# Kernel tuning notes

Measured on AMD Instinct MI355X. Metric: run time of the kernel, lower is better.

## Reference

```python
import jax, jax.numpy as jnp
import numpy as np

NUM_HEADS = 6
TAU = 1.0


def _split_heads(y, h):
    b, n, c = y.shape
    return y.reshape(b, n, h, c // h).transpose(0, 2, 1, 3)  # b h n d


def setup_inputs() -> dict:
    key = jax.random.key(0)
    B, M, C = 8, 1026, 384
    names = ["Wq1", "Wq2", "Wk1", "Wk2", "Wv1", "Wv2", "Wo"]
    ks = jax.random.split(key, len(names) + 3)
    inp = {"x": jax.random.normal(ks[0], (B, M, C), jnp.float32)}
    for i, nm in enumerate(names):
        inp[nm] = jax.random.normal(ks[i + 1], (C, C), jnp.float32) * 0.02
        inp["b" + nm[1:]] = jnp.zeros((C,), jnp.float32)
    inp["weights"] = jax.random.normal(ks[-2], (4,), jnp.float32)
    u = jax.random.uniform(ks[-1], (4,), jnp.float32, 1e-6, 1.0 - 1e-6)
    inp["gumbel_noise"] = -jnp.log(-jnp.log(u))  # fixed gumbel sample for determinism
    return inp


def reference(x, Wq1, bq1, Wq2, bq2, Wk1, bk1, Wk2, bk2,
              Wv1, bv1, Wv2, bv2, Wo, bo, weights, gumbel_noise):
    B, M, C = x.shape
    N1 = (M - 2) // 2 + 1  # N + 1, quadrant size
    h = NUM_HEADS
    d = C // h
    scale = d ** -0.5
    x1, x2 = x[:, :N1], x[:, N1:]
    q = jnp.concatenate([_split_heads(x1 @ Wq1 + bq1, h),
                         _split_heads(x2 @ Wq2 + bq2, h)], axis=2)  # b h M d
    k = jnp.concatenate([_split_heads(x1 @ Wk1 + bk1, h),
                         _split_heads(x2 @ Wk2 + bk2, h)], axis=2)
    v1 = _split_heads(x1 @ Wv1 + bv1, h)  # b h N1 d
    v2 = _split_heads(x2 @ Wv2 + bv2, h)
    attn = jnp.einsum('bhqd,bhkd->bhqk', q, k) * scale  # b h M M
    b1 = jax.nn.softmax(attn[:, :, :N1, :N1], axis=-1)
    b2 = jax.nn.softmax(attn[:, :, :N1, N1:], axis=-1)
    b3 = jax.nn.softmax(attn[:, :, N1:, :N1], axis=-1)
    b4 = jax.nn.softmax(attn[:, :, N1:, N1:], axis=-1)
    # hard gumbel-softmax gate (straight-through)
    y_soft = jax.nn.softmax((weights + gumbel_noise) / TAU)
    y_hard = jax.nn.one_hot(jnp.argmax(y_soft), 4, dtype=y_soft.dtype)
    w = y_hard + y_soft - jax.lax.stop_gradient(y_soft)
    A = w[0] * b1 + w[1] * b2 + w[2] * b3 + w[3] * b4  # b h N1 N1
    out1 = jnp.einsum('bhqk,bhkd->bhqd', A, v1)
    out2 = jnp.einsum('bhqk,bhkd->bhqd', A, v2)
    out = jnp.concatenate([out1, out2], axis=2)  # b h M d
    out = out.transpose(0, 2, 1, 3).reshape(B, M, C)
    return out @ Wo + bo
```

## Files before the change

kernel.cpp:

```cpp
#include <hip/hip_runtime.h>

typedef unsigned short u16;
typedef short v8s __attribute__((ext_vector_type(8)));
typedef float v4f __attribute__((ext_vector_type(4)));

namespace {
constexpr int kC = 384;
constexpr int kN1 = 513;
constexpr int kH = 6;
constexpr int kBH = 48;
constexpr int kRows = 4104;
constexpr int kRows2 = 8208;
constexpr int kPld = 576;
}

__device__ __forceinline__ u16 f2b(float f) {
  unsigned int u = __float_as_uint(f);
  u += 0x7fffu + ((u >> 16) & 1u);
  return (u16)(u >> 16);
}

__device__ __forceinline__ int gumbel_argmax(const float* __restrict__ w,
                                             const float* __restrict__ g) {
  float v0 = w[0] + g[0], v1 = w[1] + g[1], v2 = w[2] + g[2], v3 = w[3] + g[3];
  int j = 0;
  float m = v0;
  if (v1 > m) { m = v1; j = 1; }
  if (v2 > m) { m = v2; j = 2; }
  if (v3 > m) { m = v3; j = 3; }
  return j;
}

__global__ __launch_bounds__(256) void prep_w(
    const float* __restrict__ Wq1, const float* __restrict__ Wq2,
    const float* __restrict__ Wk1, const float* __restrict__ Wk2,
    const float* __restrict__ Wv1, const float* __restrict__ Wv2,
    const float* __restrict__ Wo, const float* __restrict__ wts,
    const float* __restrict__ gum, u16* __restrict__ Wqt,
    u16* __restrict__ Wkt, u16* __restrict__ Wv1t, u16* __restrict__ Wv2t,
    u16* __restrict__ Wot) {
  __shared__ float tb[32][33];
  const int bx = blockIdx.x;
  const int z = bx / 144, rem = bx - z * 144;
  const int c0 = (rem % 12) * 32, r0 = (rem / 12) * 32;
  const int j = gumbel_argmax(wts, gum);
  const float* src;
  u16* dst;
  switch (z) {
    case 0: src = (j < 2) ? Wq1 : Wq2; dst = Wqt; break;
    case 1: src = (j == 0 || j == 2) ? Wk1 : Wk2; dst = Wkt; break;
    case 2: src = Wv1; dst = Wv1t; break;
    case 3: src = Wv2; dst = Wv2t; break;
    default: src = Wo; dst = Wot; break;
  }
  const int tx = threadIdx.x & 31, ty = threadIdx.x >> 5;
  for (int p = 0; p < 4; ++p)
    tb[ty + p * 8][tx] = src[(size_t)(r0 + ty + p * 8) * kC + c0 + tx];
  __syncthreads();
  for (int p = 0; p < 4; ++p)
    dst[(size_t)(c0 + ty + p * 8) * kC + r0 + tx] = f2b(tb[tx][ty + p * 8]);
}

__global__ __launch_bounds__(256) void qkv_mfma(
    const float* __restrict__ x, const u16* __restrict__ Wqt,
    const u16* __restrict__ Wkt, const u16* __restrict__ Wv1t,
    const u16* __restrict__ Wv2t, const float* __restrict__ bq1,
    const float* __restrict__ bq2, const float* __restrict__ bk1,
    const float* __restrict__ bk2, const float* __restrict__ bv1,
    const float* __restrict__ bv2, const float* __restrict__ wts,
    const float* __restrict__ gum, u16* __restrict__ Qb, u16* __restrict__ Kb,
    u16* __restrict__ Vt1, u16* __restrict__ Vt2) {
  __shared__ __align__(16) u16 As[128][72];
  __shared__ __align__(16) u16 Bs[128][72];
  const int op = blockIdx.z;
  const int j = gumbel_argmax(wts, gum);
  const bool vmode = (op >= 2);
  const float* bias;
  int xoff;
  const u16* Wt;
  if (op == 0) {
    bias = (j < 2) ? bq1 : bq2; xoff = (j < 2) ? 0 : kN1; Wt = Wqt;
  } else if (op == 1) {
    const bool u1 = (j == 0 || j == 2);
    bias = u1 ? bk1 : bk2; xoff = u1 ? 0 : kN1; Wt = Wkt;
  } else if (op == 2) {
    bias = bv1; xoff = 0; Wt = Wv1t;
  } else {
    bias = bv2; xoff = kN1; Wt = Wv2t;
  }
  const int mb = vmode ? blockIdx.y : blockIdx.x;
  const int nb = vmode ? blockIdx.x : blockIdx.y;
  const int m0 = mb * 128, n0 = nb * 128;
  const int tid = threadIdx.x;
  const int lane = tid & 63, l16 = lane & 15, quad = lane >> 4;
  const int wv = tid >> 6, wr = wv >> 1, wc = wv & 1;
  const int sr = tid >> 2, sc = (tid & 3) * 16;

  v4f acc[4][4];
  const v4f z4 = {0.f, 0.f, 0.f, 0.f};
  for (int i = 0; i < 4; ++i)
    for (int n = 0; n < 4; ++n) acc[i][n] = z4;

  for (int k0 = 0; k0 < kC; k0 += 64) {
    for (int p = 0; p < 2; ++p) {
      const int r = p * 64 + sr;
      v8s v0 = {0, 0, 0, 0, 0, 0, 0, 0}, v1 = v0;
      if (!vmode) {
        const int t = m0 + r;
        if (t < kRows) {
          const int bb = t / kN1, mm = t - bb * kN1;
          const float* s = x + ((size_t)(bb * 1026 + xoff + mm)) * kC + k0 + sc;
          const float4 f0 = *(const float4*)s;
          const float4 f1 = *(const float4*)(s + 4);
          const float4 f2 = *(const float4*)(s + 8);
          const float4 f3 = *(const float4*)(s + 12);
          v0 = (v8s){(short)f2b(f0.x), (short)f2b(f0.y), (short)f2b(f0.z),
                     (short)f2b(f0.w), (short)f2b(f1.x), (short)f2b(f1.y),
                     (short)f2b(f1.z), (short)f2b(f1.w)};
          v1 = (v8s){(short)f2b(f2.x), (short)f2b(f2.y), (short)f2b(f2.z),
                     (short)f2b(f2.w), (short)f2b(f3.x), (short)f2b(f3.y),
                     (short)f2b(f3.z), (short)f2b(f3.w)};
        }
      } else {
        const u16* s = Wt + (size_t)(m0 + r) * kC + k0 + sc;
        v0 = *(const v8s*)s;
        v1 = *(const v8s*)(s + 8);
      }
      *(v8s*)&As[r][sc] = v0;
      *(v8s*)&As[r][sc + 8] = v1;
    }
    for (int p = 0; p < 2; ++p) {
      const int r = p * 64 + sr;
      v8s v0 = {0, 0, 0, 0, 0, 0, 0, 0}, v1 = v0;
      if (!vmode) {
        const u16* s = Wt + (size_t)(n0 + r) * kC + k0 + sc;
        v0 = *(const v8s*)s;
        v1 = *(const v8s*)(s + 8);
      } else {
        const int t = n0 + r;
        if (t < kRows) {
          const int bb = t / kN1, mm = t - bb * kN1;
          const float* s = x + ((size_t)(bb * 1026 + xoff + mm)) * kC + k0 + sc;
          const float4 f0 = *(const float4*)s;
          const float4 f1 = *(const float4*)(s + 4);
          const float4 f2 = *(const float4*)(s + 8);
          const float4 f3 = *(const float4*)(s + 12);
          v0 = (v8s){(short)f2b(f0.x), (short)f2b(f0.y), (short)f2b(f0.z),
                     (short)f2b(f0.w), (short)f2b(f1.x), (short)f2b(f1.y),
                     (short)f2b(f1.z), (short)f2b(f1.w)};
          v1 = (v8s){(short)f2b(f2.x), (short)f2b(f2.y), (short)f2b(f2.z),
                     (short)f2b(f2.w), (short)f2b(f3.x), (short)f2b(f3.y),
                     (short)f2b(f3.z), (short)f2b(f3.w)};
        }
      }
      *(v8s*)&Bs[r][sc] = v0;
      *(v8s*)&Bs[r][sc + 8] = v1;
    }
    __syncthreads();
    for (int ks = 0; ks < 2; ++ks) {
      v8s af[4], bfr[4];
      for (int i = 0; i < 4; ++i)
        af[i] = *(const v8s*)&As[wr * 64 + i * 16 + l16][ks * 32 + quad * 8];
      for (int n = 0; n < 4; ++n)
        bfr[n] = *(const v8s*)&Bs[wc * 64 + n * 16 + l16][ks * 32 + quad * 8];
      for (int i = 0; i < 4; ++i)
        for (int n = 0; n < 4; ++n)
          acc[i][n] = __builtin_amdgcn_mfma_f32_16x16x32_bf16(af[i], bfr[n],
                                                              acc[i][n], 0, 0, 0);
    }
    __syncthreads();
  }

  if (!vmode) {
    u16* outp = (op == 0) ? Qb : Kb;
    const float osc = (op == 0) ? 0.125f : 1.0f;
    float bv4[4];
    for (int nt = 0; nt < 4; ++nt) bv4[nt] = bias[n0 + wc * 64 + nt * 16 + l16];
    for (int i = 0; i < 4; ++i) {
      const int rowb = m0 + wr * 64 + i * 16 + quad * 4;
      for (int r = 0; r < 4; ++r) {
        const int row = rowb + r;
        if (row >= kRows) continue;
        for (int nt = 0; nt < 4; ++nt) {
          const int col = n0 + wc * 64 + nt * 16 + l16;
          outp[(size_t)row * kC + col] = f2b((acc[i][nt][r] + bv4[nt]) * osc);
        }
      }
    }
  } else {
    u16* Vt = (op == 2) ? Vt1 : Vt2;
    for (int nt = 0; nt < 4; ++nt) {
      const int t = n0 + wc * 64 + nt * 16 + l16;
      if (t >= kRows) continue;
      const int bb = t / kN1, mm = t - bb * kN1;
      for (int i = 0; i < 4; ++i) {
        const int colb = m0 + wr * 64 + i * 16 + quad * 4;
        for (int r = 0; r < 4; ++r) {
          const int col = colb + r;
          const int hh = col >> 6, d = col & 63;
          Vt[((size_t)(bb * kH + hh) * 64 + d) * kPld + mm] =
              f2b(acc[i][nt][r] + bias[col]);
        }
      }
    }
  }
}

__global__ __launch_bounds__(256) void attn_fused(const u16* __restrict__ Qb,
                                                  const u16* __restrict__ Kb,
                                                  const u16* __restrict__ Vt1,
                                                  const u16* __restrict__ Vt2,
                                                  u16* __restrict__ PRE) {
  __shared__ __align__(16) u16 Ks[64][72];
  __shared__ __align__(16) u16 Vs[128][72];
  __shared__ __align__(16) u16 Ps[4][16][72];
  const int bh = blockIdx.y;
  const int b = bh / kH, hh = bh - b * kH;
  const int q0 = blockIdx.x * 64;
  const int tid = threadIdx.x;
  const int w = tid >> 6, lane = tid & 63, l16 = lane & 15, quad = lane >> 4;
  v8s aq0, aq1;
  {
    int qr = q0 + w * 16 + l16;
    if (qr > 512) qr = 512;
    const u16* qs = Qb + ((size_t)(b * kN1 + qr)) * kC + hh * 64 + quad * 8;
    aq0 = *(const v8s*)qs;
    aq1 = *(const v8s*)(qs + 32);
  }
  const int ksr = tid >> 2, ksc = (tid & 3) * 16;
  const int vd = tid >> 1, vc = (tid & 1) * 32;
  const u16* kbase = Kb + (size_t)b * kN1 * kC + hh * 64 + ksc;
  const u16* vbase = ((vd < 64) ? (Vt1 + ((size_t)bh * 64 + vd) * kPld)
                                : (Vt2 + ((size_t)bh * 64 + (vd - 64)) * kPld)) +
                     vc;
  v8s kr0, kr1, vr0, vr1, vr2, vr3;
  {
    const u16* s = kbase + (size_t)ksr * kC;
    kr0 = *(const v8s*)s;
    kr1 = *(const v8s*)(s + 8);
    vr0 = *(const v8s*)(vbase);
    vr1 = *(const v8s*)(vbase + 8);
    vr2 = *(const v8s*)(vbase + 16);
    vr3 = *(const v8s*)(vbase + 24);
  }
  float lsum[4] = {0.f, 0.f, 0.f, 0.f};
  v4f Oacc[8];
  const v4f z4 = {0.f, 0.f, 0.f, 0.f};
  for (int n = 0; n < 8; ++n) Oacc[n] = z4;

  for (int kt = 0; kt < 9; ++kt) {
    const int k0 = kt * 64;
    __syncthreads();
    *(v8s*)&Ks[ksr][ksc] = kr0;
    *(v8s*)&Ks[ksr][ksc + 8] = kr1;
    *(v8s*)&Vs[vd][vc] = vr0;
    *(v8s*)&Vs[vd][vc + 8] = vr1;
    *(v8s*)&Vs[vd][vc + 16] = vr2;
    *(v8s*)&Vs[vd][vc + 24] = vr3;
    __syncthreads();
    if (kt < 8) {
      int ki = k0 + 64 + ksr;
      if (ki > 512) ki = 512;
      const u16* s = kbase + (size_t)ki * kC;
      kr0 = *(const v8s*)s;
      kr1 = *(const v8s*)(s + 8);
      const u16* t = vbase + k0 + 64;
      vr0 = *(const v8s*)t;
      vr1 = *(const v8s*)(t + 8);
      vr2 = *(const v8s*)(t + 16);
      vr3 = *(const v8s*)(t + 24);
    }
    v4f sacc[4];
    for (int nt = 0; nt < 4; ++nt) sacc[nt] = z4;
    for (int nt = 0; nt < 4; ++nt) {
      const v8s bk0 = *(const v8s*)&Ks[nt * 16 + l16][quad * 8];
      sacc[nt] = __builtin_amdgcn_mfma_f32_16x16x32_bf16(aq0, bk0, sacc[nt], 0, 0, 0);
      const v8s bk1 = *(const v8s*)&Ks[nt * 16 + l16][32 + quad * 8];
      sacc[nt] = __builtin_amdgcn_mfma_f32_16x16x32_bf16(aq1, bk1, sacc[nt], 0, 0, 0);
    }
    for (int r = 0; r < 4; ++r) {
      float ps = 0.f;
      for (int nt = 0; nt < 4; ++nt) {
        const int col = k0 + nt * 16 + l16;
        const float p = (col < kN1) ? __expf(sacc[nt][r]) : 0.f;
        ps += p;
        Ps[w][quad * 4 + r][nt * 16 + l16] = f2b(p);
      }
      lsum[r] += ps;
    }
    for (int kc = 0; kc < 2; ++kc) {
      const v8s ap = *(const v8s*)&Ps[w][l16][kc * 32 + quad * 8];
      for (int n = 0; n < 8; ++n) {
        const v8s bv = *(const v8s*)&Vs[n * 16 + l16][kc * 32 + quad * 8];
        Oacc[n] = __builtin_amdgcn_mfma_f32_16x16x32_bf16(ap, bv, Oacc[n], 0, 0, 0);
      }
    }
  }
  float rinv[4];
  for (int r = 0; r < 4; ++r) {
    float s = lsum[r];
    for (int o = 1; o <= 8; o <<= 1) s += __shfl_xor(s, o);
    rinv[r] = 1.f / s;
  }
  for (int n = 0; n < 8; ++n) {
    const int col = hh * 64 + (n & 3) * 16 + l16;
    const int rbase = b * 1026 + ((n < 4) ? 0 : kN1);
    for (int r = 0; r < 4; ++r) {
      const int q = q0 + w * 16 + quad * 4 + r;
      if (q >= kN1) continue;
      PRE[(size_t)(rbase + q) * kC + col] = f2b(Oacc[n][r] * rinv[r]);
    }
  }
}

__global__ __launch_bounds__(256) void out_mfma(const u16* __restrict__ PRE,
                                                const u16* __restrict__ Wot,
                                                const float* __restrict__ bo,
                                                float* __restrict__ OUT) {
  __shared__ __align__(16) u16 As[128][72];
  __shared__ __align__(16) u16 Bs[128][72];
  const int m0 = blockIdx.x * 128, n0 = blockIdx.y * 128;
  const int tid = threadIdx.x;
  const int lane = tid & 63, l16 = lane & 15, quad = lane >> 4;
  const int wv = tid >> 6, wr = wv >> 1, wc = wv & 1;
  const int sr = tid >> 2, sc = (tid & 3) * 16;
  v4f acc[4][4];
  const v4f z4 = {0.f, 0.f, 0.f, 0.f};
  for (int i = 0; i < 4; ++i)
    for (int n = 0; n < 4; ++n) acc[i][n] = z4;
  for (int k0 = 0; k0 < kC; k0 += 64) {
    for (int p = 0; p < 2; ++p) {
      const int r = p * 64 + sr;
      v8s v0 = {0, 0, 0, 0, 0, 0, 0, 0}, v1 = v0;
      const int row = m0 + r;
      if (row < kRows2) {
        const u16* s = PRE + (size_t)row * kC + k0 + sc;
        v0 = *(const v8s*)s;
        v1 = *(const v8s*)(s + 8);
      }
      *(v8s*)&As[r][sc] = v0;
      *(v8s*)&As[r][sc + 8] = v1;
      const u16* s2 = Wot + (size_t)(n0 + r) * kC + k0 + sc;
      *(v8s*)&Bs[r][sc] = *(const v8s*)s2;
      *(v8s*)&Bs[r][sc + 8] = *(const v8s*)(s2 + 8);
    }
    __syncthreads();
    for (int ks = 0; ks < 2; ++ks) {
      v8s af[4], bfr[4];
      for (int i = 0; i < 4; ++i)
        af[i] = *(const v8s*)&As[wr * 64 + i * 16 + l16][ks * 32 + quad * 8];
      for (int n = 0; n < 4; ++n)
        bfr[n] = *(const v8s*)&Bs[wc * 64 + n * 16 + l16][ks * 32 + quad * 8];
      for (int i = 0; i < 4; ++i)
        for (int n = 0; n < 4; ++n)
          acc[i][n] = __builtin_amdgcn_mfma_f32_16x16x32_bf16(af[i], bfr[n],
                                                              acc[i][n], 0, 0, 0);
    }
    __syncthreads();
  }
  float bv4[4];
  for (int nt = 0; nt < 4; ++nt) bv4[nt] = bo[n0 + wc * 64 + nt * 16 + l16];
  for (int i = 0; i < 4; ++i) {
    const int rowb = m0 + wr * 64 + i * 16 + quad * 4;
    for (int r = 0; r < 4; ++r) {
      const int row = rowb + r;
      if (row >= kRows2) continue;
      for (int nt = 0; nt < 4; ++nt) {
        const int col = n0 + wc * 64 + nt * 16 + l16;
        OUT[(size_t)row * kC + col] = acc[i][nt][r] + bv4[nt];
      }
    }
  }
}

extern "C" void kernel_launch(void* const* d_in, const int* in_sizes, int n_in,
                              void* d_out, int out_size, void* d_ws,
                              size_t ws_size, hipStream_t stream) {
  const float* x = (const float*)d_in[0];
  const float* Wq1 = (const float*)d_in[1];
  const float* bq1 = (const float*)d_in[2];
  const float* Wq2 = (const float*)d_in[3];
  const float* bq2 = (const float*)d_in[4];
  const float* Wk1 = (const float*)d_in[5];
  const float* bk1 = (const float*)d_in[6];
  const float* Wk2 = (const float*)d_in[7];
  const float* bk2 = (const float*)d_in[8];
  const float* Wv1 = (const float*)d_in[9];
  const float* bv1 = (const float*)d_in[10];
  const float* Wv2 = (const float*)d_in[11];
  const float* bv2 = (const float*)d_in[12];
  const float* Wo = (const float*)d_in[13];
  const float* bo = (const float*)d_in[14];
  const float* wts = (const float*)d_in[15];
  const float* gum = (const float*)d_in[16];

  u16* Wqt = (u16*)d_ws;
  u16* Wkt = Wqt + 147456;
  u16* Wv1t = Wkt + 147456;
  u16* Wv2t = Wv1t + 147456;
  u16* Wot = Wv2t + 147456;
  u16* Qb = Wot + 147456;
  u16* Kb = Qb + (size_t)kRows * kC;
  u16* Vt1 = Kb + (size_t)kRows * kC;
  u16* Vt2 = Vt1 + (size_t)kBH * 64 * kPld;
  u16* PRE = Vt2 + (size_t)kBH * 64 * kPld;

  prep_w<<<dim3(720), 256, 0, stream>>>(Wq1, Wq2, Wk1, Wk2, Wv1, Wv2, Wo, wts,
                                        gum, Wqt, Wkt, Wv1t, Wv2t, Wot);
  qkv_mfma<<<dim3(33, 3, 4), 256, 0, stream>>>(
      x, Wqt, Wkt, Wv1t, Wv2t, bq1, bq2, bk1, bk2, bv1, bv2, wts, gum, Qb, Kb,
      Vt1, Vt2);
  attn_fused<<<dim3(9, kBH), 256, 0, stream>>>(Qb, Kb, Vt1, Vt2, PRE);
  out_mfma<<<dim3(65, 3), 256, 0, stream>>>(PRE, Wot, bo, (float*)d_out);
}
```

Baseline: 151.0 us.

## Fuse four kernels into one cooperative persistent kernel with grid syncs

Turns the weight-prep, QKV projection, attention and output projection kernels into device phases that share one shared-memory buffer. A single cooperative kernel of 432 blocks runs them in order, with grid.sync between phases. The goal is to remove three kernel-launch gaps and their tail idle time. The cost is fixed grid sizing, grid-wide barriers, and idle blocks in phases with fewer work units. Separate kernels are kept as a fallback if the cooperative launch fails.

```diff
diff --git a/kernel.cpp b/kernel.cpp
--- a/kernel.cpp
+++ b/kernel.cpp
@@ -1,4 +1,7 @@
 #include <hip/hip_runtime.h>
+#include <hip/hip_cooperative_groups.h>
+
+namespace cg = cooperative_groups;
 
 typedef unsigned short u16;
 typedef short v8s __attribute__((ext_vector_type(8)));
@@ -12,6 +15,7 @@
 constexpr int kRows = 4104;
 constexpr int kRows2 = 8208;
 constexpr int kPld = 576;
+constexpr int kGrid = 432;
 }
 
 __device__ __forceinline__ u16 f2b(float f) {
@@ -31,19 +35,15 @@
   return j;
 }
 
-__global__ __launch_bounds__(256) void prep_w(
-    const float* __restrict__ Wq1, const float* __restrict__ Wq2,
-    const float* __restrict__ Wk1, const float* __restrict__ Wk2,
-    const float* __restrict__ Wv1, const float* __restrict__ Wv2,
-    const float* __restrict__ Wo, const float* __restrict__ wts,
-    const float* __restrict__ gum, u16* __restrict__ Wqt,
-    u16* __restrict__ Wkt, u16* __restrict__ Wv1t, u16* __restrict__ Wv2t,
-    u16* __restrict__ Wot) {
-  __shared__ float tb[32][33];
-  const int bx = blockIdx.x;
-  const int z = bx / 144, rem = bx - z * 144;
+__device__ __forceinline__ void phase_prep(
+    u16* sm, int u, const float* Wq1, const float* Wq2, const float* Wk1,
+    const float* Wk2, const float* Wv1, const float* Wv2, const float* Wo,
+    int j, u16* Wqt, u16* Wkt, u16* Wv1t, u16* Wv2t, u16* Wot) {
+  float (*tb)[33] = (float(*)[33])sm;
+  const int tid = threadIdx.x;
+  const int tx = tid & 31, ty = tid >> 5;
+  const int z = u / 144, rem = u - z * 144;
   const int c0 = (rem % 12) * 32, r0 = (rem / 12) * 32;
-  const int j = gumbel_argmax(wts, gum);
   const float* src;
   u16* dst;
   switch (z) {
@@ -53,27 +53,21 @@
     case 3: src = Wv2; dst = Wv2t; break;
     default: src = Wo; dst = Wot; break;
   }
-  const int tx = threadIdx.x & 31, ty = threadIdx.x >> 5;
   for (int p = 0; p < 4; ++p)
     tb[ty + p * 8][tx] = src[(size_t)(r0 + ty + p * 8) * kC + c0 + tx];
   __syncthreads();
   for (int p = 0; p < 4; ++p)
     dst[(size_t)(c0 + ty + p * 8) * kC + r0 + tx] = f2b(tb[tx][ty + p * 8]);
-}
-
-__global__ __launch_bounds__(256) void qkv_mfma(
-    const float* __restrict__ x, const u16* __restrict__ Wqt,
-    const u16* __restrict__ Wkt, const u16* __restrict__ Wv1t,
-    const u16* __restrict__ Wv2t, const float* __restrict__ bq1,
-    const float* __restrict__ bq2, const float* __restrict__ bk1,
-    const float* __restrict__ bk2, const float* __restrict__ bv1,
-    const float* __restrict__ bv2, const float* __restrict__ wts,
-    const float* __restrict__ gum, u16* __restrict__ Qb, u16* __restrict__ Kb,
-    u16* __restrict__ Vt1, u16* __restrict__ Vt2) {
-  __shared__ __align__(16) u16 As[128][72];
-  __shared__ __align__(16) u16 Bs[128][72];
-  const int op = blockIdx.z;
-  const int j = gumbel_argmax(wts, gum);
+  __syncthreads();
+}
+
+__device__ __forceinline__ void phase_qkv(
+    u16* sm, int op, int mb33, int nb3, const float* x, const u16* Wqt,
+    const u16* Wkt, const u16* Wv1t, const u16* Wv2t, const float* bq1,
+    const float* bq2, const float* bk1, const float* bk2, const float* bv1,
+    const float* bv2, int j, u16* Qb, u16* Kb, u16* Vt1, u16* Vt2) {
+  u16 (*As)[72] = (u16(*)[72])sm;
+  u16 (*Bs)[72] = (u16(*)[72])(sm + 9216);
   const bool vmode = (op >= 2);
   const float* bias;
   int xoff;
@@ -88,9 +82,8 @@
   } else {
     bias = bv2; xoff = kN1; Wt = Wv2t;
   }
-  const int mb = vmode ? blockIdx.y : blockIdx.x;
-  const int nb = vmode ? blockIdx.x : blockIdx.y;
-  const int m0 = mb * 128, n0 = nb * 128;
+  const int m0 = (vmode ? nb3 : mb33) * 128;
+  const int n0 = (vmode ? mb33 : nb3) * 128;
   const int tid = threadIdx.x;
   const int lane = tid & 63, l16 = lane & 15, quad = lane >> 4;
   const int wv = tid >> 6, wr = wv >> 1, wc = wv & 1;
@@ -206,17 +199,14 @@
   }
 }
 
-__global__ __launch_bounds__(256) void attn_fused(const u16* __restrict__ Qb,
-                                                  const u16* __restrict__ Kb,
-                                                  const u16* __restrict__ Vt1,
-                                                  const u16* __restrict__ Vt2,
-                                                  u16* __restrict__ PRE) {
-  __shared__ __align__(16) u16 Ks[64][72];
-  __shared__ __align__(16) u16 Vs[128][72];
-  __shared__ __align__(16) u16 Ps[4][16][72];
-  const int bh = blockIdx.y;
+__device__ __forceinline__ void phase_attn(u16* sm, int q0, int bh,
+                                           const u16* Qb, const u16* Kb,
+                                           const u16* Vt1, const u16* Vt2,
+                                           u16* PRE) {
+  u16 (*Ks)[72] = (u16(*)[72])sm;
+  u16 (*Vs)[72] = (u16(*)[72])(sm + 4608);
+  u16 (*Ps)[16][72] = (u16(*)[16][72])(sm + 13824);
   const int b = bh / kH, hh = bh - b * kH;
-  const int q0 = blockIdx.x * 64;
   const int tid = threadIdx.x;
   const int w = tid >> 6, lane = tid & 63, l16 = lane & 15, quad = lane >> 4;
   v8s aq0, aq1;
@@ -311,15 +301,14 @@
       PRE[(size_t)(rbase + q) * kC + col] = f2b(Oacc[n][r] * rinv[r]);
     }
   }
-}
-
-__global__ __launch_bounds__(256) void out_mfma(const u16* __restrict__ PRE,
-                                                const u16* __restrict__ Wot,
-                                                const float* __restrict__ bo,
-                                                float* __restrict__ OUT) {
-  __shared__ __align__(16) u16 As[128][72];
-  __shared__ __align__(16) u16 Bs[128][72];
-  const int m0 = blockIdx.x * 128, n0 = blockIdx.y * 128;
+  __syncthreads();
+}
+
+__device__ __forceinline__ void phase_out(u16* sm, int m0, int n0,
+                                          const u16* PRE, const u16* Wot,
+                                          const float* bo, float* OUT) {
+  u16 (*As)[72] = (u16(*)[72])sm;
+  u16 (*Bs)[72] = (u16(*)[72])(sm + 9216);
   const int tid = threadIdx.x;
   const int lane = tid & 63, l16 = lane & 15, quad = lane >> 4;
   const int wv = tid >> 6, wr = wv >> 1, wc = wv & 1;
@@ -371,6 +360,66 @@
       }
     }
   }
+}
+
+__global__ __launch_bounds__(256) void mega(
+    const float* x, const float* Wq1, const float* bq1, const float* Wq2,
+    const float* bq2, const float* Wk1, const float* bk1, const float* Wk2,
+    const float* bk2, const float* Wv1, const float* bv1, const float* Wv2,
+    const float* bv2, const float* Wo, const float* bo, const float* wts,
+    const float* gum, float* OUT, u16* Wqt, u16* Wkt, u16* Wv1t, u16* Wv2t,
+    u16* Wot, u16* Qb, u16* Kb, u16* Vt1, u16* Vt2, u16* PRE) {
+  cg::grid_group grid = cg::this_grid();
+  __shared__ __align__(16) u16 sm[18432];
+  const int bid = blockIdx.x;
+  const int j = gumbel_argmax(wts, gum);
+  for (int u = bid; u < 720; u += kGrid)
+    phase_prep(sm, u, Wq1, Wq2, Wk1, Wk2, Wv1, Wv2, Wo, j, Wqt, Wkt, Wv1t,
+               Wv2t, Wot);
+  __threadfence();
+  grid.sync();
+  if (bid < 396) {
+    const int op = bid / 99, rem = bid - op * 99;
+    phase_qkv(sm, op, rem % 33, rem / 33, x, Wqt, Wkt, Wv1t, Wv2t, bq1, bq2,
+              bk1, bk2, bv1, bv2, j, Qb, Kb, Vt1, Vt2);
+  }
+  __threadfence();
+  grid.sync();
+  phase_attn(sm, (bid % 9) * 64, bid / 9, Qb, Kb, Vt1, Vt2, PRE);
+  __threadfence();
+  grid.sync();
+  if (bid < 195)
+    phase_out(sm, (bid % 65) * 128, (bid / 65) * 128, PRE, Wot, bo, OUT);
+}
+
+__global__ __launch_bounds__(256) void k_prep(
+    const float* Wq1, const float* Wq2, const float* Wk1, const float* Wk2,
+    const float* Wv1, const float* Wv2, const float* Wo, const float* wts,
+    const float* gum, u16* Wqt, u16* Wkt, u16* Wv1t, u16* Wv2t, u16* Wot) {
+  __shared__ __align__(16) u16 sm[18432];
+  phase_prep(sm, blockIdx.x, Wq1, Wq2, Wk1, Wk2, Wv1, Wv2, Wo,
+             gumbel_argmax(wts, gum), Wqt, Wkt, Wv1t, Wv2t, Wot);
+}
+__global__ __launch_bounds__(256) void k_qkv(
+    const float* x, const u16* Wqt, const u16* Wkt, const u16* Wv1t,
+    const u16* Wv2t, const float* bq1, const float* bq2, const float* bk1,
+    const float* bk2, const float* bv1, const float* bv2, const float* wts,
+    const float* gum, u16* Qb, u16* Kb, u16* Vt1, u16* Vt2) {
+  __shared__ __align__(16) u16 sm[18432];
+  phase_qkv(sm, blockIdx.z, blockIdx.x, blockIdx.y, x, Wqt, Wkt, Wv1t, Wv2t,
+            bq1, bq2, bk1, bk2, bv1, bv2, gumbel_argmax(wts, gum), Qb, Kb, Vt1,
+            Vt2);
+}
+__global__ __launch_bounds__(256) void k_attn(const u16* Qb, const u16* Kb,
+                                              const u16* Vt1, const u16* Vt2,
+                                              u16* PRE) {
+  __shared__ __align__(16) u16 sm[18432];
+  phase_attn(sm, blockIdx.x * 64, blockIdx.y, Qb, Kb, Vt1, Vt2, PRE);
+}
+__global__ __launch_bounds__(256) void k_out(const u16* PRE, const u16* Wot,
+                                             const float* bo, float* OUT) {
+  __shared__ __align__(16) u16 sm[18432];
+  phase_out(sm, blockIdx.x * 128, blockIdx.y * 128, PRE, Wot, bo, OUT);
 }
 
 extern "C" void kernel_launch(void* const* d_in, const int* in_sizes, int n_in,
@@ -393,6 +442,7 @@
   const float* bo = (const float*)d_in[14];
   const float* wts = (const float*)d_in[15];
   const float* gum = (const float*)d_in[16];
+  float* OUT = (float*)d_out;
 
   u16* Wqt = (u16*)d_ws;
   u16* Wkt = Wqt + 147456;
@@ -405,11 +455,18 @@
   u16* Vt2 = Vt1 + (size_t)kBH * 64 * kPld;
   u16* PRE = Vt2 + (size_t)kBH * 64 * kPld;
 
-  prep_w<<<dim3(720), 256, 0, stream>>>(Wq1, Wq2, Wk1, Wk2, Wv1, Wv2, Wo, wts,
-                                        gum, Wqt, Wkt, Wv1t, Wv2t, Wot);
-  qkv_mfma<<<dim3(33, 3, 4), 256, 0, stream>>>(
-      x, Wqt, Wkt, Wv1t, Wv2t, bq1, bq2, bk1, bk2, bv1, bv2, wts, gum, Qb, Kb,
-      Vt1, Vt2);
-  attn_fused<<<dim3(9, kBH), 256, 0, stream>>>(Qb, Kb, Vt1, Vt2, PRE);
-  out_mfma<<<dim3(65, 3), 256, 0, stream>>>(PRE, Wot, bo, (float*)d_out);
-}
+  void* args[] = {&x,   &Wq1, &bq1, &Wq2,  &bq2,  &Wk1, &bk1, &Wk2, &bk2, &Wv1,
+                  &bv1, &Wv2, &bv2, &Wo,   &bo,   &wts, &gum, &OUT, &Wqt, &Wkt,
+                  &Wv1t, &Wv2t, &Wot, &Qb, &Kb, &Vt1, &Vt2, &PRE};
+  const hipError_t err = hipLaunchCooperativeKernel(
+      (const void*)mega, dim3(kGrid), dim3(256), args, 0, stream);
+  if (err != hipSuccess) {
+    k_prep<<<dim3(720), 256, 0, stream>>>(Wq1, Wq2, Wk1, Wk2, Wv1, Wv2, Wo,
+                                          wts, gum, Wqt, Wkt, Wv1t, Wv2t, Wot);
+    k_qkv<<<dim3(33, 3, 4), 256, 0, stream>>>(x, Wqt, Wkt, Wv1t, Wv2t, bq1,
+                                              bq2, bk1, bk2, bv1, bv2, wts,
+                                              gum, Qb, Kb, Vt1, Vt2);
+    k_attn<<<dim3(9, kBH), 256, 0, stream>>>(Qb, Kb, Vt1, Vt2, PRE);
+    k_out<<<dim3(65, 3), 256, 0, stream>>>(PRE, Wot, bo, OUT);
+  }
+}
```

Result: slower. 481.2 us (+218.7%).
